# Performance work log

Measured on AMD Instinct MI355X. Metric: run time of the kernel, lower is better.

## Reference

```python
import jax, jax.numpy as jnp
import numpy as np

KERNEL_SIZE = 15  # module init kwarg


def _box_filter(x, k):
    c = x.shape[1]
    dn = ('NCHW', 'OIHW', 'NCHW')
    kh = jnp.ones((c, 1, k, 1), x.dtype)
    kw = jnp.ones((c, 1, 1, k), x.dtype)
    p = k // 2
    x = jax.lax.conv_general_dilated(x, kh, (1, 1), [(p, p), (0, 0)],
                                     dimension_numbers=dn, feature_group_count=c)
    x = jax.lax.conv_general_dilated(x, kw, (1, 1), [(0, 0), (p, p)],
                                     dimension_numbers=dn, feature_group_count=c)
    return x


def setup_inputs() -> dict:
    key = jax.random.key(0)
    k1, k2 = jax.random.split(key)
    b, c, h, w = 8, 19, 512, 1024
    input = jax.random.normal(k1, (b, c, h, w), dtype=jnp.float32)
    target = jax.random.randint(k2, (b, 1, h, w), 0, c, dtype=jnp.int32)
    return {"input": input, "target": target}


def reference(input, target):
    k = KERNEL_SIZE
    c = input.shape[1]
    # one-hot mask [b,c,h,w] (equivalent to the per-class (target==i) cat loop)
    mask = jnp.transpose(jax.nn.one_hot(target[:, 0], c, dtype=input.dtype), (0, 3, 1, 2))
    # per-class local count of same-class pixels in a k x k window
    count = _box_filter(mask, k)
    # since mask is one-hot, sum over channels picks the count at the true class (>= 1)
    wsum = jnp.sum(count * mask, axis=1, keepdims=True)  # [b,1,h,w]
    weight = (k * k) / wsum
    # gather the input score at the true class and weight it
    out = jnp.sum(input * mask, axis=1, keepdims=True) * (-weight)
    return jnp.mean(out)
```

## Files before the change

kernel.cpp:

```cpp
#include <hip/hip_runtime.h>
#include <stdint.h>

#define BB 8
#define CC 19
#define HH 512
#define WW 1024
#define KK 15
#define RR 7
#define TH 8
#define NROWS (TH + 2*RR)
#define P_DW 34
#define HW (HH*WW)
#define NPIX (BB*HH*WW)
#define NBLK (BB*(HH/TH))

__global__ __launch_bounds__(256) void wce_main(const float* __restrict__ in,
                                                const int* __restrict__ tg,
                                                float* __restrict__ part) {
  __shared__ uint32_t P[CC][NROWS][P_DW];
  __shared__ uint32_t Cc[TH][256];
  __shared__ float wpart[4];
  const int tid = threadIdx.x;
  const int blk = blockIdx.x;
  const int bb  = blk >> 6;
  const int h0  = (blk & 63) * TH;

  uint32_t* pflat = &P[0][0][0];
  #pragma unroll 4
  for (int i = tid; i < CC*NROWS*P_DW; i += 256) pflat[i] = 0;
  __syncthreads();

  for (int idx = tid; idx < NROWS*256; idx += 256) {
    const int r = idx >> 8, d = idx & 255;
    const int h = h0 - RR + r;
    if (h >= 0 && h < HH) {
      const int4 t4 = *reinterpret_cast<const int4*>(&tg[(bb*HH + h)*WW + d*4]);
      const int rc = r - RR;
      if (rc >= 0 && rc < TH)
        Cc[rc][d] = (uint32_t)(t4.x & 0xff)        | ((uint32_t)(t4.y & 0xff) << 8)
                  | ((uint32_t)(t4.z & 0xff) << 16) | ((uint32_t)(t4.w & 0xff) << 24);
      const int col = d * 4;
      const int dw  = 1 + (col >> 5);
      const int b   = col & 31;
      atomicOr(&P[t4.x][r][dw], 1u << (b + 0));
      atomicOr(&P[t4.y][r][dw], 1u << (b + 1));
      atomicOr(&P[t4.z][r][dw], 1u << (b + 2));
      atomicOr(&P[t4.w][r][dw], 1u << (b + 3));
    }
  }
  __syncthreads();

  const int g = tid;

  uint32_t c4s[TH];
  float x[TH][4];
  #pragma unroll
  for (int s = 0; s < TH; ++s) {
    const uint32_t c4 = Cc[s][g];
    c4s[s] = c4;
    const int base = bb*CC*HW + (h0 + s)*WW + 4*g;
    x[s][0] = in[base + (int)( c4        & 0xff)*HW + 0];
    x[s][1] = in[base + (int)((c4 >> 8)  & 0xff)*HW + 1];
    x[s][2] = in[base + (int)((c4 >> 16) & 0xff)*HW + 2];
    x[s][3] = in[base + (int)((c4 >> 24) & 0xff)*HW + 3];
  }

  float acc = 0.0f;
  #pragma unroll
  for (int s = 0; s < TH; ++s) {
    const uint32_t c4 = c4s[s];
    #pragma unroll
    for (int i = 0; i < 4; ++i) {
      const int c  = (int)((c4 >> (8*i)) & 0xff);
      const int lb = 4*g + i - 7;
      const int q  = (lb >> 5) + 1;
      const int sh = lb & 31;
      const uint32_t* pr = &P[c][s][q];
      int cn = 0;
      #pragma unroll
      for (int wr = 0; wr < KK; ++wr) {
        const uint32_t lo = pr[0], hi = pr[1];
        cn += __popc(__builtin_amdgcn_alignbit(hi, lo, sh) & 0x7fffu);
        pr += P_DW;
      }
      acc += x[s][i] * (225.0f / (float)cn);
    }
  }

  #pragma unroll
  for (int off = 32; off > 0; off >>= 1) acc += __shfl_down(acc, off, 64);
  const int lane = tid & 63, wv = tid >> 6;
  if (lane == 0) wpart[wv] = acc;
  __syncthreads();
  if (tid == 0) part[blk] = wpart[0] + wpart[1] + wpart[2] + wpart[3];
}

__global__ __launch_bounds__(256) void wce_reduce(const float* __restrict__ part,
                                                  float* __restrict__ out, int n) {
  __shared__ float wpart[4];
  float a = 0.0f;
  for (int i = threadIdx.x; i < n; i += 256) a += part[i];
  #pragma unroll
  for (int off = 32; off > 0; off >>= 1) a += __shfl_down(a, off, 64);
  const int lane = threadIdx.x & 63, wv = threadIdx.x >> 6;
  if (lane == 0) wpart[wv] = a;
  __syncthreads();
  if (threadIdx.x == 0) {
    const float tot = wpart[0] + wpart[1] + wpart[2] + wpart[3];
    out[0] = -tot / (float)NPIX;
  }
}

extern "C" void kernel_launch(void* const* d_in, const int* in_sizes, int n_in,
                              void* d_out, int out_size, void* d_ws, size_t ws_size,
                              hipStream_t stream) {
  const float* in = (const float*)d_in[0];
  const int*   tg = (const int*)d_in[1];
  float* out  = (float*)d_out;
  float* part = (float*)d_ws;

  wce_main<<<NBLK, 256, 0, stream>>>(in, tg, part);
  wce_reduce<<<1, 256, 0, stream>>>(part, out, NBLK);
}
```

Before: 58.62 us.

## Split tiles in half-width and sort pixels by class to coalesce gathered input loads

Each block now covers an 8x512 tile instead of 8x1024, which doubles the grid and adds halo columns to the class bitmask. The per-pixel weights go into shared memory, and a per-class histogram plus counting sort reorders pixel indices by class. The final pass then reads the input mostly within one channel plane at a time, so the scattered channel gather becomes closer to coalesced access. In exchange it adds shared-memory atomics, several extra barriers, a serial prefix sum and more shared memory per block, which may lower occupancy.

```diff
diff --git a/kernel.cpp b/kernel.cpp
--- a/kernel.cpp
+++ b/kernel.cpp
@@ -8,40 +8,51 @@
 #define KK 15
 #define RR 7
 #define TH 8
+#define WHALF 512
 #define NROWS (TH + 2*RR)
-#define P_DW 34
+#define P_DW 18
+#define NK 136
 #define HW (HH*WW)
 #define NPIX (BB*HH*WW)
-#define NBLK (BB*(HH/TH))
+#define NBLK (BB*(HH/TH)*2)
+#define PXB (TH*WHALF)
 
 __global__ __launch_bounds__(256) void wce_main(const float* __restrict__ in,
                                                 const int* __restrict__ tg,
                                                 float* __restrict__ part) {
   __shared__ uint32_t P[CC][NROWS][P_DW];
-  __shared__ uint32_t Cc[TH][256];
+  __shared__ uint32_t Cc[TH][WHALF/4];
+  __shared__ float    wbuf[PXB];
+  __shared__ uint16_t sidx[PXB];
+  __shared__ uint32_t hist[CC][8];
+  __shared__ uint32_t off[CC];
   __shared__ float wpart[4];
   const int tid = threadIdx.x;
   const int blk = blockIdx.x;
-  const int bb  = blk >> 6;
-  const int h0  = (blk & 63) * TH;
+  const int bb  = blk >> 7;
+  const int rem = blk & 127;
+  const int h0  = (rem >> 1) * TH;
+  const int w0  = (rem & 1) * WHALF;
 
   uint32_t* pflat = &P[0][0][0];
   #pragma unroll 4
   for (int i = tid; i < CC*NROWS*P_DW; i += 256) pflat[i] = 0;
+  if (tid < CC*8) (&hist[0][0])[tid] = 0;
   __syncthreads();
 
-  for (int idx = tid; idx < NROWS*256; idx += 256) {
-    const int r = idx >> 8, d = idx & 255;
+  for (int idx = tid; idx < NROWS*NK; idx += 256) {
+    const int r = idx / NK;
+    const int k = idx - r*NK;
     const int h = h0 - RR + r;
-    if (h >= 0 && h < HH) {
-      const int4 t4 = *reinterpret_cast<const int4*>(&tg[(bb*HH + h)*WW + d*4]);
+    const int wg = w0 - 16 + 4*k;
+    if (h >= 0 && h < HH && wg >= 0 && wg < WW) {
+      const int4 t4 = *reinterpret_cast<const int4*>(&tg[(bb*HH + h)*WW + wg]);
       const int rc = r - RR;
-      if (rc >= 0 && rc < TH)
-        Cc[rc][d] = (uint32_t)(t4.x & 0xff)        | ((uint32_t)(t4.y & 0xff) << 8)
-                  | ((uint32_t)(t4.z & 0xff) << 16) | ((uint32_t)(t4.w & 0xff) << 24);
-      const int col = d * 4;
-      const int dw  = 1 + (col >> 5);
-      const int b   = col & 31;
+      if (rc >= 0 && rc < TH && k >= 4 && k < 132)
+        Cc[rc][k-4] = (uint32_t)(t4.x & 0xff)        | ((uint32_t)(t4.y & 0xff) << 8)
+                    | ((uint32_t)(t4.z & 0xff) << 16) | ((uint32_t)(t4.w & 0xff) << 24);
+      const int dw = k >> 3;
+      const int b  = (4*k) & 31;
       atomicOr(&P[t4.x][r][dw], 1u << (b + 0));
       atomicOr(&P[t4.y][r][dw], 1u << (b + 1));
       atomicOr(&P[t4.z][r][dw], 1u << (b + 2));
@@ -50,30 +61,18 @@
   }
   __syncthreads();
 
-  const int g = tid;
+  const int g  = tid & 127;
+  const int sb = (tid >> 7) << 2;
 
-  uint32_t c4s[TH];
-  float x[TH][4];
   #pragma unroll
-  for (int s = 0; s < TH; ++s) {
+  for (int so = 0; so < 4; ++so) {
+    const int s = sb + so;
     const uint32_t c4 = Cc[s][g];
-    c4s[s] = c4;
-    const int base = bb*CC*HW + (h0 + s)*WW + 4*g;
-    x[s][0] = in[base + (int)( c4        & 0xff)*HW + 0];
-    x[s][1] = in[base + (int)((c4 >> 8)  & 0xff)*HW + 1];
-    x[s][2] = in[base + (int)((c4 >> 16) & 0xff)*HW + 2];
-    x[s][3] = in[base + (int)((c4 >> 24) & 0xff)*HW + 3];
-  }
-
-  float acc = 0.0f;
-  #pragma unroll
-  for (int s = 0; s < TH; ++s) {
-    const uint32_t c4 = c4s[s];
     #pragma unroll
     for (int i = 0; i < 4; ++i) {
       const int c  = (int)((c4 >> (8*i)) & 0xff);
-      const int lb = 4*g + i - 7;
-      const int q  = (lb >> 5) + 1;
+      const int lb = 4*g + i + 9;
+      const int q  = lb >> 5;
       const int sh = lb & 31;
       const uint32_t* pr = &P[c][s][q];
       int cn = 0;
@@ -83,12 +82,52 @@
         cn += __popc(__builtin_amdgcn_alignbit(hi, lo, sh) & 0x7fffu);
         pr += P_DW;
       }
-      acc += x[s][i] * (225.0f / (float)cn);
+      wbuf[(s << 9) + 4*g + i] = 225.0f / (float)cn;
+      atomicAdd(&hist[c][tid & 7], 1u);
     }
+  }
+  __syncthreads();
+
+  if (tid < CC) {
+    uint32_t t = 0;
+    #pragma unroll
+    for (int k = 0; k < 8; ++k) t += hist[tid][k];
+    hist[tid][0] = t;
+  }
+  __syncthreads();
+  if (tid == 0) {
+    uint32_t run = 0;
+    for (int c = 0; c < CC; ++c) { off[c] = run; run += hist[c][0]; }
+  }
+  __syncthreads();
+
+  #pragma unroll
+  for (int so = 0; so < 4; ++so) {
+    const int s = sb + so;
+    const uint32_t c4 = Cc[s][g];
+    #pragma unroll
+    for (int i = 0; i < 4; ++i) {
+      const int c = (int)((c4 >> (8*i)) & 0xff);
+      const uint32_t pos = atomicAdd(&off[c], 1u);
+      sidx[pos] = (uint16_t)((s << 9) + 4*g + i);
+    }
+  }
+  __syncthreads();
+
+  const int gbase = bb*CC*HW + h0*WW + w0;
+  float acc = 0.0f;
+  #pragma unroll 4
+  for (int i = 0; i < PXB/256; ++i) {
+    const int j  = (i << 8) + tid;
+    const int p  = (int)sidx[j];
+    const int s  = p >> 9, wl = p & 511;
+    const uint32_t cw = Cc[s][wl >> 2];
+    const int c  = (int)((cw >> ((wl & 3)*8)) & 0xff);
+    acc += wbuf[p] * in[gbase + s*WW + wl + c*HW];
   }
 
   #pragma unroll
-  for (int off = 32; off > 0; off >>= 1) acc += __shfl_down(acc, off, 64);
+  for (int o = 32; o > 0; o >>= 1) acc += __shfl_down(acc, o, 64);
   const int lane = tid & 63, wv = tid >> 6;
   if (lane == 0) wpart[wv] = acc;
   __syncthreads();
@@ -101,7 +140,7 @@
   float a = 0.0f;
   for (int i = threadIdx.x; i < n; i += 256) a += part[i];
   #pragma unroll
-  for (int off = 32; off > 0; off >>= 1) a += __shfl_down(a, off, 64);
+  for (int o = 32; o > 0; o >>= 1) a += __shfl_down(a, o, 64);
   const int lane = threadIdx.x & 63, wv = threadIdx.x >> 6;
   if (lane == 0) wpart[wv] = a;
   __syncthreads();
```

Result: slower. 73.97 us (+26.2%).
